# Optimization experiments

Measured on AMD Instinct MI355X. Metric: run time of the kernel, lower is better.

Reference implementation:

```python
import jax, jax.numpy as jnp
import numpy as np

N_NODES = 100000
N_EDGES = 1600000
N_RELS = 8
IN_F, HID_F, OUT_F = 64, 64, 32


def rgcn_conv(x, src, dst, etype, W, root, bias, num_nodes, num_rels):
    """PyG RGCNConv: out[i] = x[i]@root + bias + sum_r mean_{j in N_r(i)} x[j]@W_r."""
    E = src.shape[0]
    seg = dst * num_rels + etype  # combined (node, relation) segment id
    cnt = jax.ops.segment_sum(jnp.ones((E,), x.dtype), seg,
                              num_segments=num_nodes * num_rels)
    norm = 1.0 / jnp.maximum(cnt[seg], 1.0)  # per-edge 1/|N_r(dst)|
    h = jnp.einsum('ni,rio->rno', x, W)      # [R, N, O] relation-transformed feats
    msg = h[etype, src] * norm[:, None]      # gather per edge, normalize
    agg = jax.ops.segment_sum(msg, dst, num_segments=num_nodes)
    return agg + x @ root + bias


def setup_inputs() -> dict:
    key = jax.random.key(0)
    ks = jax.random.split(key, 10)
    x = jax.random.normal(ks[0], (N_NODES, IN_F), dtype=jnp.float32)
    edge_index = jax.random.randint(ks[1], (2, N_EDGES), 0, N_NODES, dtype=jnp.int64)
    edge_type = jax.random.randint(ks[2], (N_EDGES,), 0, N_RELS, dtype=jnp.int64)
    s1 = 1.0 / np.sqrt(IN_F)
    s2 = 1.0 / np.sqrt(HID_F)
    W1 = jax.random.uniform(ks[3], (N_RELS, IN_F, HID_F), jnp.float32, -s1, s1)
    root1 = jax.random.uniform(ks[4], (IN_F, HID_F), jnp.float32, -s1, s1)
    b1 = jnp.zeros((HID_F,), jnp.float32)
    W2 = jax.random.uniform(ks[5], (N_RELS, HID_F, OUT_F), jnp.float32, -s2, s2)
    root2 = jax.random.uniform(ks[6], (HID_F, OUT_F), jnp.float32, -s2, s2)
    b2 = jnp.zeros((OUT_F,), jnp.float32)
    return {"x": x, "edge_index": edge_index, "edge_type": edge_type,
            "W1": W1, "root1": root1, "b1": b1,
            "W2": W2, "root2": root2, "b2": b2}


def reference(x, edge_index, edge_type, W1, root1, b1, W2, root2, b2):
    src, dst = edge_index[0], edge_index[1]
    h = rgcn_conv(x, src, dst, edge_type, W1, root1, b1, N_NODES, N_RELS)
    h = jax.nn.relu(h)
    out = rgcn_conv(h, src, dst, edge_type, W2, root2, b2, N_NODES, N_RELS)
    return out
```

## Files before the change

### kernel.cpp

```cpp
#include <hip/hip_runtime.h>
#include <hip/hip_bf16.h>

#define N_NODES 100000
#define N_EDGES 1600000
#define N_RELS  8
#define IN_F    64
#define HID_F   64
#define OUT_F   32
#define NSEG    (N_NODES * N_RELS)
#define SCAN_EPB 1024
#define SCAN_NB  ((NSEG + SCAN_EPB - 1) / SCAN_EPB)

typedef __attribute__((ext_vector_type(8))) short short8;
typedef __attribute__((ext_vector_type(4))) float f32x4;

__device__ __forceinline__ float b2f(unsigned short u) {
    return __uint_as_float(((unsigned)u) << 16);
}
__device__ __forceinline__ unsigned short f2b(float f) {
    unsigned u = __float_as_uint(f);
    u += 0x7FFFu + ((u >> 16) & 1u);
    return (unsigned short)(u >> 16);
}

#define PREP_W1 (576 * 64)
#define PREP_W2 (576 * 32)
#define PREP_CVT (N_NODES * 64 / 4)
#define PREP_TOT (PREP_W1 + PREP_W2 + PREP_CVT)

__global__ void k_hist(const int* __restrict__ dst, const int* __restrict__ et,
                       int* __restrict__ cnt, int* __restrict__ rank,
                       const float* __restrict__ W1, const float* __restrict__ root1,
                       const float* __restrict__ W2, const float* __restrict__ root2,
                       const float* __restrict__ x,
                       ushort* __restrict__ Wt1b, ushort* __restrict__ Wt2b,
                       ushort* __restrict__ xb) {
    const int e = blockIdx.x * 256 + threadIdx.x;
    const int gsz = gridDim.x * 256;
    for (int j = e; j < PREP_TOT; j += gsz) {
        if (j < PREP_W1) {
            int o = j / 576, k = j - o * 576;
            float v = (k < 512) ? W1[k * 64 + o] : root1[(k - 512) * 64 + o];
            Wt1b[j] = f2b(v);
        } else if (j < PREP_W1 + PREP_W2) {
            int j2 = j - PREP_W1;
            int o = j2 / 576, k = j2 - o * 576;
            float v = (k < 512) ? W2[k * 32 + o] : root2[(k - 512) * 32 + o];
            Wt2b[j2] = f2b(v);
        } else {
            int j2 = j - PREP_W1 - PREP_W2;
            float4 v = *(const float4*)(x + (size_t)j2 * 4);
            ushort4 u;
            u.x = f2b(v.x); u.y = f2b(v.y); u.z = f2b(v.z); u.w = f2b(v.w);
            *(ushort4*)(xb + (size_t)j2 * 4) = u;
        }
    }
    if (e < N_EDGES) {
        int seg = dst[e] * N_RELS + et[e];
        rank[e] = atomicAdd(&cnt[seg], 1);
    }
}

__global__ void k_scanA(const int* __restrict__ cnt, int* __restrict__ bsums) {
    __shared__ int red[256];
    int t = threadIdx.x;
    int base = blockIdx.x * SCAN_EPB + t * 4;
    int s = 0;
    #pragma unroll
    for (int j = 0; j < 4; ++j) {
        int idx = base + j;
        if (idx < NSEG) s += cnt[idx];
    }
    red[t] = s;
    __syncthreads();
    for (int st = 128; st > 0; st >>= 1) {
        if (t < st) red[t] += red[t + st];
        __syncthreads();
    }
    if (t == 0) bsums[blockIdx.x] = red[0];
}

__global__ void k_scanC(const int* __restrict__ cnt, const int* __restrict__ bsums,
                        int* __restrict__ offs) {
    __shared__ int red[256];
    __shared__ int ts[256];
    int t = threadIdx.x;

    int partial = 0;
    #pragma unroll
    for (int jj = 0; jj < 4; ++jj) {
        int j = t + jj * 256;
        if (j < SCAN_NB && j < (int)blockIdx.x) partial += bsums[j];
    }
    red[t] = partial;
    __syncthreads();
    for (int st = 128; st > 0; st >>= 1) {
        if (t < st) red[t] += red[t + st];
        __syncthreads();
    }
    const int base0 = red[0];

    int base = blockIdx.x * SCAN_EPB + t * 4;
    int v[4];
    int local = 0;
    #pragma unroll
    for (int j = 0; j < 4; ++j) {
        int idx = base + j;
        v[j] = (idx < NSEG) ? cnt[idx] : 0;
        local += v[j];
    }
    ts[t] = local;
    __syncthreads();
    for (int off = 1; off < 256; off <<= 1) {
        int x = (t >= off) ? ts[t - off] : 0;
        __syncthreads();
        ts[t] += x;
        __syncthreads();
    }
    int run = base0 + (ts[t] - local);
    #pragma unroll
    for (int j = 0; j < 4; ++j) {
        int idx = base + j;
        if (idx < NSEG) offs[idx] = run;
        run += v[j];
    }
}

__global__ void k_scat(const int* __restrict__ src, const int* __restrict__ dst,
                       const int* __restrict__ et, const int* __restrict__ offs,
                       const int* __restrict__ rank, int* __restrict__ ssrc) {
    int e = blockIdx.x * 256 + threadIdx.x;
    if (e < N_EDGES) {
        int r = et[e];
        int d = dst[e];
        int seg = d * N_RELS + r;
        ssrc[offs[seg] + rank[e]] = (src[e] << 8) | ((d & 15) << 4) | r;
    }
}

template <int NOUT, bool RELU, typename OutT>
__global__ __launch_bounds__(512, 4) void k_layer(
        const ushort* __restrict__ xb, const int* __restrict__ offs,
        const int* __restrict__ cnt, const int* __restrict__ ssrc,
        const ushort* __restrict__ Wtb, const float* __restrict__ bias,
        OutT* __restrict__ out) {
    constexpr int NT = NOUT / 16;
    constexpr int S  = 8 / NT;
    __shared__ __align__(16) union {
        float  a32[128][64];
        ushort a16[16][584];
    } U;
    __shared__ float invT[128];
    __shared__ f32x4 pc[6][64];

    const int tid = threadIdx.x;
    const int w = tid >> 6;
    const int f = tid & 63;
    const int node0 = blockIdx.x * 16;

    const int t = w % NT, q = w / NT;
    constexpr int cbase = 18 / S, crem = 18 % S;
    const int cs = q * cbase + (q < crem ? q : crem);
    const int ce = cs + cbase + (q < crem ? 1 : 0);
    const int n0 = t * 16;
    const ushort* bptr = Wtb + (n0 + (f & 15)) * 576 + ((f >> 4) * 8);
    short8 bcur = *(const short8*)(bptr + cs * 32);

    float* S32 = &U.a32[0][0];
    {
        f32x4 z = (f32x4){0.0f, 0.0f, 0.0f, 0.0f};
        #pragma unroll
        for (int k = 0; k < 4; ++k)
            *(f32x4*)(S32 + tid * 16 + k * 4) = z;
        if (tid < 128) {
            int c = cnt[node0 * 8 + tid];
            invT[tid] = 1.0f / (float)(c > 0 ? c : 1);
        }
    }

    int ov = 0, cv = 0;
    if (f < 16) {
        ov = offs[(node0 + w * 2) * N_RELS + f];
        cv = cnt [(node0 + w * 2) * N_RELS + f];
    }
    __syncthreads();

    for (int nd = 0; nd < 2; ++nd) {
        const int m = w * 2 + nd;
        const int s0 = __builtin_amdgcn_readlane(ov, nd * 8);
        const int ct = __builtin_amdgcn_readlane(ov, nd * 8 + 7)
                     + __builtin_amdgcn_readlane(cv, nd * 8 + 7) - s0;

        float running = 0.0f;
        int prl = 15;

        for (int cb = 0; cb < ct; cb += 64) {
            int n = ct - cb;
            if (n > 64) n = 64;
            int pk = 15;
            if (f < n) pk = ssrc[s0 + cb + f];
            for (int e = 0; e < n; e += 16) {
                int pv[16];
                float xv[16];
                #pragma unroll
                for (int i = 0; i < 16; ++i)
                    pv[i] = __builtin_amdgcn_readlane(pk, e + i);
                #pragma unroll
                for (int i = 0; i < 16; ++i)
                    xv[i] = b2f(xb[(size_t)((unsigned)pv[i] >> 8) * 64 + f]);
                #pragma unroll
                for (int i = 0; i < 16; ++i) {
                    const int rl = pv[i] & 15;
                    if (rl != prl) {
                        if (prl < 8)
                            U.a32[(m << 3) + prl][f] = running;
                        running = 0.0f;
                        prl = rl;
                    }
                    running += xv[i];
                }
            }
        }
        if (prl < 8)
            U.a32[(m << 3) + prl][f] = running;
    }
    __syncthreads();

    float rv[16];
    {
        const int row = tid >> 2;
        const int fb = (tid & 3) * 16;
        const float inv = invT[row];
        #pragma unroll
        for (int k = 0; k < 4; ++k) {
            f32x4 v = *(f32x4*)(S32 + row * 64 + fb + k * 4);
            rv[k * 4 + 0] = v.x * inv; rv[k * 4 + 1] = v.y * inv;
            rv[k * 4 + 2] = v.z * inv; rv[k * 4 + 3] = v.w * inv;
        }
    }
    __syncthreads();
    {
        const int row = tid >> 2;
        const int nib = row >> 3, rel = row & 7;
        const int fb = (tid & 3) * 16;
        ushort* dp = &U.a16[nib][rel * 64 + fb];
        short8 o0, o1;
        #pragma unroll
        for (int k = 0; k < 8; ++k) o0[k] = (short)f2b(rv[k]);
        #pragma unroll
        for (int k = 0; k < 8; ++k) o1[k] = (short)f2b(rv[8 + k]);
        *(short8*)dp = o0;
        *(short8*)(dp + 8) = o1;
        const int m = tid >> 5, f2 = (tid & 31) * 2;
        uint xr = *(const uint*)(xb + (size_t)(node0 + m) * 64 + f2);
        *(uint*)&U.a16[m][512 + f2] = xr;
    }
    __syncthreads();

    f32x4 acc = (f32x4){0.0f, 0.0f, 0.0f, 0.0f};
    const ushort* aptr = &U.a16[f & 15][(f >> 4) * 8];
    for (int c = cs; c < ce; ++c) {
        short8 bnext = bcur;
        if (c + 1 < ce) bnext = *(const short8*)(bptr + (c + 1) * 32);
        short8 af = *(const short8*)(aptr + c * 32);
        acc = __builtin_amdgcn_mfma_f32_16x16x32_bf16(af, bcur, acc, 0, 0, 0);
        bcur = bnext;
    }

    if (q > 0) pc[w - NT][f] = acc;
    __syncthreads();
    if (q == 0) {
        #pragma unroll
        for (int j = 1; j < S; ++j) {
            f32x4 p = pc[t + NT * (j - 1)][f];
            acc.x += p.x; acc.y += p.y; acc.z += p.z; acc.w += p.w;
        }
        const int col = f & 15;
        const float bs = bias[n0 + col];
        const int mrow = (f >> 4) * 4;
        #pragma unroll
        for (int i = 0; i < 4; ++i) {
            float v = acc[i] + bs;
            if (RELU) v = fmaxf(v, 0.0f);
            size_t oi = (size_t)(node0 + mrow + i) * NOUT + n0 + col;
            if constexpr (sizeof(OutT) == 2) out[oi] = (OutT)f2b(v);
            else                             out[oi] = (OutT)v;
        }
    }
}

extern "C" void kernel_launch(void* const* d_in, const int* in_sizes, int n_in,
                              void* d_out, int out_size, void* d_ws, size_t ws_size,
                              hipStream_t stream) {
    const float* x     = (const float*)d_in[0];
    const int*   ei    = (const int*)d_in[1];
    const int*   et    = (const int*)d_in[2];
    const float* W1    = (const float*)d_in[3];
    const float* root1 = (const float*)d_in[4];
    const float* b1    = (const float*)d_in[5];
    const float* W2    = (const float*)d_in[6];
    const float* root2 = (const float*)d_in[7];
    const float* b2    = (const float*)d_in[8];
    float* out = (float*)d_out;

    const int* src = ei;
    const int* dst = ei + N_EDGES;

    char* ws = (char*)d_ws;
    int*    cnt   = (int*)(ws);
    int*    offs  = (int*)(ws + (size_t)NSEG * 4);
    int*    bsums = (int*)(ws + (size_t)NSEG * 8);
    int*    ssrc  = (int*)(ws + (size_t)NSEG * 8 + 4096);
    ushort* xb    = (ushort*)(ws + (size_t)NSEG * 8 + 4096 + (size_t)N_EDGES * 4);
    ushort* h1b   = (ushort*)((char*)xb + (size_t)N_NODES * 64 * 2);
    int*    rank  = (int*)h1b;
    ushort* Wt1b  = (ushort*)((char*)h1b + (size_t)N_NODES * 64 * 2);
    ushort* Wt2b  = (ushort*)((char*)Wt1b + (size_t)PREP_W1 * 2);

    (void)hipMemsetAsync(cnt, 0, (size_t)NSEG * 4, stream);

    int eb = (N_EDGES + 255) / 256;
    k_hist<<<eb, 256, 0, stream>>>(dst, et, cnt, rank,
                                   W1, root1, W2, root2, x, Wt1b, Wt2b, xb);
    k_scanA<<<SCAN_NB, 256, 0, stream>>>(cnt, bsums);
    k_scanC<<<SCAN_NB, 256, 0, stream>>>(cnt, bsums, offs);
    k_scat<<<eb, 256, 0, stream>>>(src, dst, et, offs, rank, ssrc);

    k_layer<64, true, ushort><<<N_NODES / 16, 512, 0, stream>>>(
        xb, offs, cnt, ssrc, Wt1b, b1, h1b);
    k_layer<32, false, float><<<N_NODES / 16, 512, 0, stream>>>(
        h1b, offs, cnt, ssrc, Wt2b, b2, out);
}
```

Before: 358.7 us.

## Balance edge aggregation across waves with LDS atomics instead of per-node assignment

Edge aggregation previously gave each wave two fixed destination nodes, so waves holding high-degree nodes set the block's pace. Each wave now takes an equal contiguous slice of the block's sorted edge range and flushes its per-segment partial sums into the shared accumulator with LDS atomicAdd, using the packed node-low-bits and relation field as the segment key. The shared tile is padded to 68 columns and the partial-accumulator buffer is aliased into the union to save LDS. The cost is atomic traffic at slice boundaries and the padding bookkeeping.

```diff
diff --git a/kernel.cpp b/kernel.cpp
--- a/kernel.cpp
+++ b/kernel.cpp
@@ -147,11 +147,13 @@
     constexpr int NT = NOUT / 16;
     constexpr int S  = 8 / NT;
     __shared__ __align__(16) union {
-        float  a32[128][64];
+        float  a32[128 * 68];
         ushort a16[16][584];
     } U;
     __shared__ float invT[128];
-    __shared__ f32x4 pc[6][64];
+
+    float* S32 = U.a32;
+    f32x4* pc = (f32x4*)((char*)&U + 18688);
 
     const int tid = threadIdx.x;
     const int w = tid >> 6;
@@ -166,39 +168,33 @@
     const ushort* bptr = Wtb + (n0 + (f & 15)) * 576 + ((f >> 4) * 8);
     short8 bcur = *(const short8*)(bptr + cs * 32);
 
-    float* S32 = &U.a32[0][0];
     {
         f32x4 z = (f32x4){0.0f, 0.0f, 0.0f, 0.0f};
         #pragma unroll
         for (int k = 0; k < 4; ++k)
-            *(f32x4*)(S32 + tid * 16 + k * 4) = z;
+            *(f32x4*)(S32 + (tid + k * 512) * 4) = z;
+        S32[8192 + tid] = 0.0f;
         if (tid < 128) {
             int c = cnt[node0 * 8 + tid];
             invT[tid] = 1.0f / (float)(c > 0 ? c : 1);
         }
     }
-
-    int ov = 0, cv = 0;
-    if (f < 16) {
-        ov = offs[(node0 + w * 2) * N_RELS + f];
-        cv = cnt [(node0 + w * 2) * N_RELS + f];
-    }
-    __syncthreads();
-
-    for (int nd = 0; nd < 2; ++nd) {
-        const int m = w * 2 + nd;
-        const int s0 = __builtin_amdgcn_readlane(ov, nd * 8);
-        const int ct = __builtin_amdgcn_readlane(ov, nd * 8 + 7)
-                     + __builtin_amdgcn_readlane(cv, nd * 8 + 7) - s0;
-
+    const int start = offs[node0 * 8];
+    const int end = (node0 + 16 >= N_NODES) ? N_EDGES : offs[(node0 + 16) * 8];
+    __syncthreads();
+
+    {
+        const int tot = end - start;
+        const int ebase = tot >> 3, erem = tot & 7;
+        const int ms = start + w * ebase + (w < erem ? w : erem);
+        const int me = ms + ebase + (w < erem ? 1 : 0);
         float running = 0.0f;
-        int prl = 15;
-
-        for (int cb = 0; cb < ct; cb += 64) {
-            int n = ct - cb;
+        int pseg = 255;
+        for (int cb = ms; cb < me; cb += 64) {
+            int n = me - cb;
             if (n > 64) n = 64;
-            int pk = 15;
-            if (f < n) pk = ssrc[s0 + cb + f];
+            int pk = 0xFF;
+            if (f < n) pk = ssrc[cb + f];
             for (int e = 0; e < n; e += 16) {
                 int pv[16];
                 float xv[16];
@@ -210,19 +206,23 @@
                     xv[i] = b2f(xb[(size_t)((unsigned)pv[i] >> 8) * 64 + f]);
                 #pragma unroll
                 for (int i = 0; i < 16; ++i) {
-                    const int rl = pv[i] & 15;
-                    if (rl != prl) {
-                        if (prl < 8)
-                            U.a32[(m << 3) + prl][f] = running;
+                    const int sg = pv[i] & 255;
+                    if (sg != pseg) {
+                        if (pseg != 255) {
+                            const int row = ((pseg >> 4) << 3) | (pseg & 7);
+                            atomicAdd(&S32[row * 68 + f], running);
+                        }
                         running = 0.0f;
-                        prl = rl;
+                        pseg = sg;
                     }
                     running += xv[i];
                 }
             }
         }
-        if (prl < 8)
-            U.a32[(m << 3) + prl][f] = running;
+        if (pseg != 255) {
+            const int row = ((pseg >> 4) << 3) | (pseg & 7);
+            atomicAdd(&S32[row * 68 + f], running);
+        }
     }
     __syncthreads();
 
@@ -233,7 +233,7 @@
         const float inv = invT[row];
         #pragma unroll
         for (int k = 0; k < 4; ++k) {
-            f32x4 v = *(f32x4*)(S32 + row * 64 + fb + k * 4);
+            f32x4 v = *(f32x4*)(S32 + row * 68 + fb + k * 4);
             rv[k * 4 + 0] = v.x * inv; rv[k * 4 + 1] = v.y * inv;
             rv[k * 4 + 2] = v.z * inv; rv[k * 4 + 3] = v.w * inv;
         }
@@ -267,12 +267,12 @@
         bcur = bnext;
     }
 
-    if (q > 0) pc[w - NT][f] = acc;
+    if (q > 0) pc[(w - NT) * 64 + f] = acc;
     __syncthreads();
     if (q == 0) {
         #pragma unroll
         for (int j = 1; j < S; ++j) {
-            f32x4 p = pc[t + NT * (j - 1)][f];
+            f32x4 p = pc[(t + NT * (j - 1)) * 64 + f];
             acc.x += p.x; acc.y += p.y; acc.z += p.z; acc.w += p.w;
         }
         const int col = f & 15;
```

New measurement: 715.5 us. 1.99x slower.
